# Performance work log

Measured on AMD Instinct MI355X. Metric: run time of the kernel, lower is better.

The kernel has to match this reference:

```python
import jax, jax.numpy as jnp
import numpy as np

DIM_IN = 30
DIM_Z = 32
TEMP = DIM_Z ** 0.5
N1, N2 = 2000, 4000


def setup_inputs() -> dict:
    key = jax.random.key(0)
    ks = jax.random.split(key, 16)
    s = 0.05
    f32 = jnp.float32
    return {
        "lm_X": jax.random.normal(ks[0], (N1, DIM_IN), f32),
        "lm_Y": jax.random.normal(ks[1], (N1, 2), f32),
        "tg_X": jax.random.normal(ks[2], (N2, DIM_IN), f32),
        "tg_Y": jax.random.normal(ks[3], (N2, 2), f32),
        "lm_delay": jax.random.uniform(ks[4], (N1,), f32),
        "tg_delay": jax.random.uniform(ks[5], (N2,), f32),
        "gamma_1": jnp.ones((1, 1), f32),
        "gamma_2": jnp.ones((1, 1), f32),
        "gamma_3": jnp.ones((1, 1), f32),
        "alpha": jnp.ones((1, 1), f32),
        "beta": jnp.zeros((1, 1), f32),
        "att_qw": jax.random.normal(ks[6], (DIM_IN, DIM_Z), f32) * s,
        "att_qb": jnp.zeros((DIM_Z,), f32),
        "att_kw": jax.random.normal(ks[7], (DIM_IN, DIM_Z), f32) * s,
        "att_kb": jnp.zeros((DIM_Z,), f32),
        "att_vw": jax.random.normal(ks[8], (DIM_IN + 2, DIM_Z), f32) * s,
        "att_vb": jnp.zeros((DIM_Z,), f32),
        "w1_w": jax.random.normal(ks[9], (DIM_IN + 2, DIM_IN + 2), f32) * s,
        "w1_b": jnp.zeros((DIM_IN + 2,), f32),
        "w2_w": jax.random.normal(ks[10], (DIM_IN + 2, DIM_IN + 2), f32) * s,
        "w2_b": jnp.zeros((DIM_IN + 2,), f32),
        "pred_qw": jax.random.normal(ks[11], (DIM_IN * 3 + 4, DIM_Z), f32) * s,
        "pred_qb": jnp.zeros((DIM_Z,), f32),
        "pred_kw": jax.random.normal(ks[12], (DIM_IN, DIM_Z), f32) * s,
        "pred_kb": jnp.zeros((DIM_Z,), f32),
        "pred_vw": jax.random.normal(ks[13], (2, 2), f32) * s,
        "pred_vb": jnp.zeros((2,), f32),
    }


def reference(lm_X, lm_Y, tg_X, tg_Y, lm_delay, tg_delay,
              gamma_1, gamma_2, gamma_3, alpha, beta,
              att_qw, att_qb, att_kw, att_kb, att_vw, att_vb,
              w1_w, w1_b, w2_w, w2_b,
              pred_qw, pred_qb, pred_kw, pred_kb, pred_vw, pred_vb):
    n1, n2 = lm_X.shape[0], tg_X.shape[0]
    n = n1 + n2 + 1
    dt = lm_X.dtype

    lm_feature = jnp.concatenate([lm_X, lm_Y], axis=1)                      # [N1, 32]
    tg_feature_0 = jnp.concatenate([tg_X, jnp.zeros((n2, 2), dt)], axis=1)  # [N2, 32]
    router_0 = jnp.mean(lm_feature, axis=0, keepdims=True)                  # [1, 32]
    all_feature_0 = jnp.concatenate([lm_feature, tg_feature_0, router_0], axis=0)

    # SimpleAttention1 (attribute similarity): log-softmax scores, exp -> softmax weights
    q = tg_X @ att_qw + att_qb
    k = lm_X @ att_kw + att_kb
    log_attn = jax.nn.log_softmax((q / TEMP) @ k.T, axis=-1)                # [N2, N1]
    attribute_score = jnp.exp(log_attn)

    delay_score = jnp.exp(-gamma_1 * (alpha * lm_delay + beta)).reshape(n1)
    rou2tar_0 = jnp.exp(-gamma_2 * (alpha * tg_delay + beta)).reshape(n2)

    # hop 1: dense star-graph adjacency, degree-normalized propagation
    adj0 = jnp.eye(n, dtype=dt)
    adj0 = adj0.at[n1:n1 + n2, :n1].set(attribute_score)
    adj0 = adj0.at[-1, :n1].set(delay_score)
    adj0 = adj0.at[n1:n1 + n2, -1].set(rou2tar_0)
    deg0 = jnp.sum(adj0, axis=1)
    step1 = ((adj0 / deg0[:, None]) @ all_feature_0) @ w1_w + w1_b          # D^-1 A X W1
    tg_feature_1 = step1[n1:n1 + n2]
    router_1 = step1[-1:].reshape(1, -1)

    # hop 2: router -> target only
    rou2tar_1 = jnp.exp(-gamma_3 * (alpha * tg_delay + beta)).reshape(n2)
    adj1 = jnp.eye(n, dtype=dt)
    adj1 = adj1.at[n1:n1 + n2, -1].set(rou2tar_1)
    all_feature_1 = jnp.concatenate([lm_feature, tg_feature_1, router_1], axis=0)
    deg1 = jnp.sum(adj1, axis=1)
    step2 = ((adj1 / deg1[:, None]) @ all_feature_1) @ w2_w + w2_b
    tg_feature_2 = step2[n1:n1 + n2]

    final_tg_feature = jnp.concatenate([tg_X, tg_feature_1, tg_feature_2], axis=-1)  # [N2, 94]

    # SimpleAttention2 (collaborative mlp): softmax attention over landmark locations
    pq = final_tg_feature @ pred_qw + pred_qb
    pk = lm_X @ pred_kw + pred_kb
    pv = lm_Y @ pred_vw + pred_vb
    pattn = jax.nn.softmax((pq / TEMP) @ pk.T, axis=-1)                     # [N2, N1]
    y_pred = pattn @ pv                                                     # [N2, 2]
    return y_pred, final_tg_feature
```

## Files before the change

kernel.cpp:

```cpp
#include <hip/hip_runtime.h>

#define N1v 2000
#define N2v 4000
#define DIN 30
#define DZ 32
#define DQ 94
#define INV_TEMP 0.17677669529663687f

__device__ __forceinline__ float wave_reduce_sum(float v) {
#pragma unroll
    for (int off = 32; off; off >>= 1) v += __shfl_xor(v, off, 64);
    return v;
}
__device__ __forceinline__ float rlane(float v, int l) {
    return __uint_as_float(__builtin_amdgcn_readlane(__float_as_uint(v), l));
}

__global__ __launch_bounds__(256) void prep_kernel(
    const float* __restrict__ lm_X, const float* __restrict__ lm_Y,
    const float* __restrict__ lm_delay, const float* __restrict__ tg_X,
    const float* __restrict__ att_qw, const float* __restrict__ att_qb,
    const float* __restrict__ att_kw, const float* __restrict__ att_kb,
    const float* __restrict__ pred_kw, const float* __restrict__ pred_kb,
    const float* __restrict__ pred_vw, const float* __restrict__ pred_vb,
    const float* __restrict__ gamma_1, const float* __restrict__ alpha,
    const float* __restrict__ beta,
    float* __restrict__ lm_feature, float* __restrict__ k_t,
    float* __restrict__ pk_t, float* __restrict__ pv,
    float* __restrict__ pS, float* __restrict__ pW, float* __restrict__ pSd,
    float* __restrict__ q_ws)
{
    __shared__ float sh_x[8][DIN];
    __shared__ float sh_k[DZ][9];
    __shared__ float sh_p[DZ][9];
    __shared__ float sh_s[8][DZ];
    __shared__ float sh_w[8][DZ];
    __shared__ float sh_d[8];
    const int t = threadIdx.x;

    if (blockIdx.x >= 250) {
        const int base = (blockIdx.x - 250) * 8;
        if (t < 8 * DIN) sh_x[t / DIN][t % DIN] = tg_X[base * DIN + t];
        __syncthreads();
        const int ty = t >> 5, c2 = t & 31;
        float acc = att_qb[c2];
#pragma unroll
        for (int d = 0; d < DIN; ++d) acc += sh_x[ty][d] * att_qw[d * DZ + c2];
        q_ws[(base + ty) * DZ + c2] = acc * INV_TEMP;
        return;
    }

    const int base = blockIdx.x * 8;
    if (t < 8 * DIN) sh_x[t / DIN][t % DIN] = lm_X[base * DIN + t];
    __syncthreads();
    const int ty = t >> 5, c = t & 31;
    const int row = base + ty;
    float kacc = att_kb[c], pacc = pred_kb[c];
#pragma unroll
    for (int d = 0; d < DIN; ++d) {
        float x = sh_x[ty][d];
        kacc += x * att_kw[d * DZ + c];
        pacc += x * pred_kw[d * DZ + c];
    }
    sh_k[c][ty] = kacc;
    sh_p[c][ty] = pacc;
    float f = (c < DIN) ? sh_x[ty][c] : lm_Y[row * 2 + (c - DIN)];
    lm_feature[row * DZ + c] = f;
    float ds = __expf(-gamma_1[0] * (alpha[0] * lm_delay[row] + beta[0]));
    sh_s[ty][c] = f;
    sh_w[ty][c] = ds * f;
    if (c == 0) sh_d[ty] = ds;
    if (c < 2) {
        pv[row * 2 + c] = lm_Y[row * 2] * pred_vw[c] +
                          lm_Y[row * 2 + 1] * pred_vw[2 + c] + pred_vb[c];
    }
    __syncthreads();
    const int oc = t >> 3, orow = t & 7;
    k_t[oc * N1v + base + orow] = sh_k[oc][orow];
    pk_t[oc * N1v + base + orow] = sh_p[oc][orow];
    if (t < DZ) {
        float S = 0.f, W = 0.f;
#pragma unroll
        for (int g = 0; g < 8; ++g) { S += sh_s[g][t]; W += sh_w[g][t]; }
        pS[blockIdx.x * DZ + t] = S;
        pW[blockIdx.x * DZ + t] = W;
    }
    if (t == DZ) {
        float Sd = 0.f;
#pragma unroll
        for (int g = 0; g < 8; ++g) Sd += sh_d[g];
        pSd[blockIdx.x] = Sd;
    }
}

__global__ __launch_bounds__(256) void attn1_kernel(
    const float* __restrict__ q_ws, const float* __restrict__ k_t,
    const float* __restrict__ lm_feature,
    const float* __restrict__ pS, const float* __restrict__ pW,
    const float* __restrict__ pSd,
    const float* __restrict__ w1_w, const float* __restrict__ w1_b,
    float* __restrict__ a1den, float* __restrict__ a1agg,
    float* __restrict__ router_0, float* __restrict__ router_1)
{
    __shared__ __align__(16) float e_lds[4][8][288];
    __shared__ float rps[8][DZ];
    __shared__ float rpw[8][DZ];
    __shared__ float rpd[8];
    __shared__ float rhr[DZ];
    const int tid = threadIdx.x;

    if (blockIdx.x == 1000) {
        const int c = tid & 31, g = tid >> 5;
        float S = 0.f, W = 0.f, Sd = 0.f;
        for (int b = g; b < 250; b += 8) {
            S += pS[b * DZ + c];
            W += pW[b * DZ + c];
            if (c == 0) Sd += pSd[b];
        }
        rps[g][c] = S; rpw[g][c] = W;
        if (c == 0) rpd[g] = Sd;
        __syncthreads();
        if (tid < DZ) {
            float S2 = 0.f, W2 = 0.f, Sd2 = 0.f;
#pragma unroll
            for (int g2 = 0; g2 < 8; ++g2) { S2 += rps[g2][tid]; W2 += rpw[g2][tid]; Sd2 += rpd[g2]; }
            float r0 = S2 / (float)N1v;
            router_0[tid] = r0;
            rhr[tid] = (r0 + W2) / (1.f + Sd2);
        }
        __syncthreads();
        if (tid < DZ) {
            float acc = w1_b[tid];
#pragma unroll
            for (int d = 0; d < DZ; ++d) acc += rhr[d] * w1_w[d * DZ + tid];
            router_1[tid] = acc;
        }
        return;
    }

    const int wv = tid >> 6;
    const int lane = tid & 63;
    const int half = lane >> 5, c = lane & 31;
    const int tg = blockIdx.x >> 3;
    const int chunk = blockIdx.x & 7;
    const int t0 = tg * 32 + wv * 8;

    float qreg[4];
#pragma unroll
    for (int p = 0; p < 4; ++p)
        qreg[p] = q_ws[(t0 + 2 * p + half) * DZ + c];

    const int r0 = lane * 4;
    const int tb = chunk << 8;
    const int j = tb + r0;
    const int rld = (j <= N1v - 4) ? j : (N1v - 4);
    const bool dead = (j >= N1v);

    float s[8][4] = {};
    const float* kp = k_t + rld;
#pragma unroll 8
    for (int cc = 0; cc < DZ; ++cc) {
        float4 kt = *(const float4*)(kp + cc * N1v);
#pragma unroll
        for (int p = 0; p < 4; ++p) {
            float qa = rlane(qreg[p], cc);
            float qb = rlane(qreg[p], 32 + cc);
            s[2*p][0] += qa*kt.x; s[2*p][1] += qa*kt.y; s[2*p][2] += qa*kt.z; s[2*p][3] += qa*kt.w;
            s[2*p+1][0] += qb*kt.x; s[2*p+1][1] += qb*kt.y; s[2*p+1][2] += qb*kt.z; s[2*p+1][3] += qb*kt.w;
        }
    }
    if (dead) {
#pragma unroll
        for (int t = 0; t < 8; ++t)
#pragma unroll
            for (int k = 0; k < 4; ++k) s[t][k] = -1e30f;
    }

    const int wbase = (r0 & 7) * 36 + (r0 >> 3);
    float den[8];
#pragma unroll
    for (int t = 0; t < 8; ++t) {
        float e0 = __expf(s[t][0]), e1 = __expf(s[t][1]);
        float e2 = __expf(s[t][2]), e3 = __expf(s[t][3]);
        den[t] = (e0 + e1) + (e2 + e3);
        e_lds[wv][t][wbase      ] = e0;
        e_lds[wv][t][wbase +  36] = e1;
        e_lds[wv][t][wbase +  72] = e2;
        e_lds[wv][t][wbase + 108] = e3;
    }

    const int rg = lane >> 3, cq = lane & 7;
    const int ebase = rg * 36;
    const float* lmp = lm_feature + (tb + rg) * DZ + cq * 4;
    float agg[8][4] = {};
#pragma unroll 2
    for (int p4 = 0; p4 < 8; ++p4) {
        float4 ev[8];
#pragma unroll
        for (int t = 0; t < 8; ++t)
            ev[t] = *(const float4*)&e_lds[wv][t][ebase + p4 * 4];
#pragma unroll
        for (int k = 0; k < 4; ++k) {
            float4 lmv = *(const float4*)(lmp + ((p4 * 4 + k) << 8));
#pragma unroll
            for (int t = 0; t < 8; ++t) {
                float e = (k == 0) ? ev[t].x : (k == 1) ? ev[t].y : (k == 2) ? ev[t].z : ev[t].w;
                agg[t][0] += e*lmv.x; agg[t][1] += e*lmv.y;
                agg[t][2] += e*lmv.z; agg[t][3] += e*lmv.w;
            }
        }
    }

#pragma unroll
    for (int t = 0; t < 8; ++t) {
#pragma unroll
        for (int off = 8; off <= 32; off <<= 1)
#pragma unroll
            for (int k = 0; k < 4; ++k) agg[t][k] += __shfl_xor(agg[t][k], off, 64);
        den[t] = wave_reduce_sum(den[t]);
    }
    if (lane < 8) {
#pragma unroll
        for (int t = 0; t < 8; ++t) {
            float4 av = {agg[t][0], agg[t][1], agg[t][2], agg[t][3]};
            *(float4*)&a1agg[((t0 + t) * 8 + chunk) * DZ + lane * 4] = av;
        }
    }
    float dout = 0.f;
#pragma unroll
    for (int t = 0; t < 8; ++t)
        if (lane == t) dout = den[t];
    if (lane < 8)
        a1den[(t0 + lane) * 8 + chunk] = dout;
}

__global__ __launch_bounds__(256) void merge1_kernel(
    const float* __restrict__ tg_X, const float* __restrict__ tg_delay,
    const float* __restrict__ w1_w, const float* __restrict__ w1_b,
    const float* __restrict__ w2_w, const float* __restrict__ w2_b,
    const float* __restrict__ pred_qw, const float* __restrict__ pred_qb,
    const float* __restrict__ gamma_2, const float* __restrict__ gamma_3,
    const float* __restrict__ alpha, const float* __restrict__ beta,
    const float* __restrict__ router_0, const float* __restrict__ router_1,
    const float* __restrict__ a1den, const float* __restrict__ a1agg,
    float* __restrict__ ftf_out, float* __restrict__ pq_ws)
{
    const int t = threadIdx.x;
    const int wv = t >> 6;
    const int lane = t & 63;
    const int half = lane >> 5, cc2 = lane & 31;
    const int i = blockIdx.x * 8 + wv * 2 + half;

    float dsum = 0.f, asum = 0.f;
#pragma unroll
    for (int w = 0; w < 8; ++w) {
        dsum += a1den[i * 8 + w];
        asum += a1agg[(i * 8 + w) * DZ + cc2];
    }

    float xr = (cc2 < DIN) ? tg_X[i * DIN + cc2] : 0.f;
    const float al = alpha[0], be = beta[0];
    float td = tg_delay[i];
    float r2t0 = __expf(-gamma_2[0] * (al * td + be));
    float r2t1 = __expf(-gamma_3[0] * (al * td + be));
    float h0 = (xr + asum / dsum + r2t0 * router_0[cc2]) / (2.f + r2t0);
    float tf1 = w1_b[cc2];
#pragma unroll 8
    for (int d = 0; d < DZ; ++d) {
        float hv = half ? rlane(h0, 32 + d) : rlane(h0, d);
        tf1 += hv * w1_w[d * DZ + cc2];
    }
    float h1 = (tf1 + r2t1 * router_1[cc2]) / (1.f + r2t1);
    float tf2 = w2_b[cc2];
#pragma unroll 8
    for (int d = 0; d < DZ; ++d) {
        float hv = half ? rlane(h1, 32 + d) : rlane(h1, d);
        tf2 += hv * w2_w[d * DZ + cc2];
    }
    if (cc2 < DIN) ftf_out[i * DQ + cc2] = xr;
    ftf_out[i * DQ + DIN + cc2] = tf1;
    ftf_out[i * DQ + DIN + DZ + cc2] = tf2;
    float pq = pred_qb[cc2];
#pragma unroll 8
    for (int d = 0; d < DIN; ++d) {
        float hv = half ? rlane(xr, 32 + d) : rlane(xr, d);
        pq += hv * pred_qw[d * DZ + cc2];
    }
#pragma unroll 8
    for (int d = 0; d < DZ; ++d) {
        float hv = half ? rlane(tf1, 32 + d) : rlane(tf1, d);
        pq += hv * pred_qw[(DIN + d) * DZ + cc2];
    }
#pragma unroll 8
    for (int d = 0; d < DZ; ++d) {
        float hv = half ? rlane(tf2, 32 + d) : rlane(tf2, d);
        pq += hv * pred_qw[(DIN + DZ + d) * DZ + cc2];
    }
    pq_ws[i * DZ + cc2] = pq * INV_TEMP;
}

__global__ __launch_bounds__(256) void attn2_kernel(
    const float* __restrict__ pq_ws, const float* __restrict__ pk_t,
    const float* __restrict__ pv, float* __restrict__ a2p)
{
    __shared__ __align__(16) float4 red[4][8][64];
    const int wv = threadIdx.x >> 6;
    const int lane = threadIdx.x & 63;
    const int half = lane >> 5, c = lane & 31;
    const int tg = blockIdx.x >> 3;
    const int chunk = blockIdx.x & 7;
    const int t0 = tg * 32 + wv * 8;

    float qreg[4];
#pragma unroll
    for (int p = 0; p < 4; ++p)
        qreg[p] = pq_ws[(t0 + 2 * p + half) * DZ + c];

    const int r0 = lane * 4;
    const int tb = chunk << 8;
    const int j = tb + r0;
    const int rld = (j <= N1v - 4) ? j : (N1v - 4);
    const bool dead = (j >= N1v);

    float s[8][4] = {};
    const float* kp = pk_t + rld;
#pragma unroll 8
    for (int cc = 0; cc < DZ; ++cc) {
        float4 kt = *(const float4*)(kp + cc * N1v);
#pragma unroll
        for (int p = 0; p < 4; ++p) {
            float qa = rlane(qreg[p], cc);
            float qb = rlane(qreg[p], 32 + cc);
            s[2*p][0] += qa*kt.x; s[2*p][1] += qa*kt.y; s[2*p][2] += qa*kt.z; s[2*p][3] += qa*kt.w;
            s[2*p+1][0] += qb*kt.x; s[2*p+1][1] += qb*kt.y; s[2*p+1][2] += qb*kt.z; s[2*p+1][3] += qb*kt.w;
        }
    }
    if (dead) {
#pragma unroll
        for (int t = 0; t < 8; ++t)
#pragma unroll
            for (int k = 0; k < 4; ++k) s[t][k] = -1e30f;
    }

    float4 pva = *(const float4*)(pv + 2 * rld);
    float4 pvb = *(const float4*)(pv + 2 * rld + 4);
#pragma unroll
    for (int t = 0; t < 8; ++t) {
        float e0 = __expf(s[t][0]), e1 = __expf(s[t][1]);
        float e2 = __expf(s[t][2]), e3 = __expf(s[t][3]);
        float d2 = (e0 + e1) + (e2 + e3);
        float ya = e0*pva.x + e1*pva.z + e2*pvb.x + e3*pvb.z;
        float yb = e0*pva.y + e1*pva.w + e2*pvb.y + e3*pvb.w;
        red[wv][t][lane] = make_float4(d2, ya, yb, 0.f);
    }

    const int rt = lane >> 3, rk = lane & 7;
    float4 acc = red[wv][rt][rk];
#pragma unroll
    for (int k = 1; k < 8; ++k) {
        float4 v = red[wv][rt][rk + 8 * k];
        acc.x += v.x; acc.y += v.y; acc.z += v.z;
    }
#pragma unroll
    for (int off = 1; off <= 4; off <<= 1) {
        acc.x += __shfl_xor(acc.x, off, 64);
        acc.y += __shfl_xor(acc.y, off, 64);
        acc.z += __shfl_xor(acc.z, off, 64);
    }
    if (rk == 0)
        ((float4*)a2p)[chunk * N2v + t0 + rt] = acc;
}

__global__ __launch_bounds__(256) void merge2_kernel(
    const float* __restrict__ a2p, float* __restrict__ y_out)
{
    const int t = blockIdx.x * 256 + threadIdx.x;
    if (t >= N2v) return;
    float D = 0.f, Y0 = 0.f, Y1 = 0.f;
#pragma unroll
    for (int w = 0; w < 8; ++w) {
        float4 v = ((const float4*)a2p)[w * N2v + t];
        D += v.x; Y0 += v.y; Y1 += v.z;
    }
    y_out[2 * t] = Y0 / D;
    y_out[2 * t + 1] = Y1 / D;
}

extern "C" void kernel_launch(void* const* d_in, const int* in_sizes, int n_in,
                              void* d_out, int out_size, void* d_ws, size_t ws_size,
                              hipStream_t stream) {
    const float* lm_X     = (const float*)d_in[0];
    const float* lm_Y     = (const float*)d_in[1];
    const float* tg_X     = (const float*)d_in[2];
    const float* lm_delay = (const float*)d_in[4];
    const float* tg_delay = (const float*)d_in[5];
    const float* gamma_1  = (const float*)d_in[6];
    const float* gamma_2  = (const float*)d_in[7];
    const float* gamma_3  = (const float*)d_in[8];
    const float* alpha    = (const float*)d_in[9];
    const float* beta     = (const float*)d_in[10];
    const float* att_qw   = (const float*)d_in[11];
    const float* att_qb   = (const float*)d_in[12];
    const float* att_kw   = (const float*)d_in[13];
    const float* att_kb   = (const float*)d_in[14];
    const float* w1_w     = (const float*)d_in[17];
    const float* w1_b     = (const float*)d_in[18];
    const float* w2_w     = (const float*)d_in[19];
    const float* w2_b     = (const float*)d_in[20];
    const float* pred_qw  = (const float*)d_in[21];
    const float* pred_qb  = (const float*)d_in[22];
    const float* pred_kw  = (const float*)d_in[23];
    const float* pred_kb  = (const float*)d_in[24];
    const float* pred_vw  = (const float*)d_in[25];
    const float* pred_vb  = (const float*)d_in[26];

    float* ws          = (float*)d_ws;
    float* k_t         = ws;
    float* pk_t        = ws + 64000;
    float* lm_feature  = ws + 128000;
    float* pv          = ws + 192000;
    float* pS          = ws + 196000;
    float* pW          = ws + 204000;
    float* pSd         = ws + 212000;
    float* router_0    = ws + 212256;
    float* router_1    = ws + 212288;
    float* q_ws        = ws + 212320;
    float* pq_ws       = ws + 340320;
    float* a1den       = ws + 468320;
    float* a1agg       = ws + 500320;
    float* a2p         = ws + 1524320;

    float* y_out   = (float*)d_out;
    float* ftf_out = y_out + 2 * N2v;

    prep_kernel<<<250 + N2v / 8, 256, 0, stream>>>(
        lm_X, lm_Y, lm_delay, tg_X, att_qw, att_qb, att_kw, att_kb,
        pred_kw, pred_kb, pred_vw, pred_vb, gamma_1, alpha, beta,
        lm_feature, k_t, pk_t, pv, pS, pW, pSd, q_ws);

    attn1_kernel<<<1001, 256, 0, stream>>>(
        q_ws, k_t, lm_feature, pS, pW, pSd, w1_w, w1_b,
        a1den, a1agg, router_0, router_1);

    merge1_kernel<<<500, 256, 0, stream>>>(
        tg_X, tg_delay, w1_w, w1_b, w2_w, w2_b,
        pred_qw, pred_qb, gamma_2, gamma_3, alpha, beta,
        router_0, router_1, a1den, a1agg, ftf_out, pq_ws);

    attn2_kernel<<<1000, 256, 0, stream>>>(
        pq_ws, pk_t, pv, a2p);

    merge2_kernel<<<16, 256, 0, stream>>>(a2p, y_out);
}
```

Before: 59.16 us.

## Fuse merge1 into attn2, recomputing target query per chunk block

The merge1 kernel is folded into attn2. Each attn2 block recomputes the GCN hop features and prediction queries for its 32 targets into shared memory, and only chunk 0 writes final_tg_feature. This removes one kernel launch and the pq_ws global round trip. In exchange, the merge work is done redundantly 8 times, once per landmark chunk, which lengthens each attn2 block's prologue.

```diff
diff --git a/kernel.cpp b/kernel.cpp
--- a/kernel.cpp
+++ b/kernel.cpp
@@ -234,7 +234,7 @@
         a1den[(t0 + lane) * 8 + chunk] = dout;
 }
 
-__global__ __launch_bounds__(256) void merge1_kernel(
+__global__ __launch_bounds__(256) void attn2_kernel(
     const float* __restrict__ tg_X, const float* __restrict__ tg_delay,
     const float* __restrict__ w1_w, const float* __restrict__ w1_b,
     const float* __restrict__ w2_w, const float* __restrict__ w2_b,
@@ -243,78 +243,78 @@
     const float* __restrict__ alpha, const float* __restrict__ beta,
     const float* __restrict__ router_0, const float* __restrict__ router_1,
     const float* __restrict__ a1den, const float* __restrict__ a1agg,
-    float* __restrict__ ftf_out, float* __restrict__ pq_ws)
-{
-    const int t = threadIdx.x;
-    const int wv = t >> 6;
-    const int lane = t & 63;
-    const int half = lane >> 5, cc2 = lane & 31;
-    const int i = blockIdx.x * 8 + wv * 2 + half;
-
-    float dsum = 0.f, asum = 0.f;
-#pragma unroll
-    for (int w = 0; w < 8; ++w) {
-        dsum += a1den[i * 8 + w];
-        asum += a1agg[(i * 8 + w) * DZ + cc2];
-    }
-
-    float xr = (cc2 < DIN) ? tg_X[i * DIN + cc2] : 0.f;
-    const float al = alpha[0], be = beta[0];
-    float td = tg_delay[i];
-    float r2t0 = __expf(-gamma_2[0] * (al * td + be));
-    float r2t1 = __expf(-gamma_3[0] * (al * td + be));
-    float h0 = (xr + asum / dsum + r2t0 * router_0[cc2]) / (2.f + r2t0);
-    float tf1 = w1_b[cc2];
-#pragma unroll 8
-    for (int d = 0; d < DZ; ++d) {
-        float hv = half ? rlane(h0, 32 + d) : rlane(h0, d);
-        tf1 += hv * w1_w[d * DZ + cc2];
-    }
-    float h1 = (tf1 + r2t1 * router_1[cc2]) / (1.f + r2t1);
-    float tf2 = w2_b[cc2];
-#pragma unroll 8
-    for (int d = 0; d < DZ; ++d) {
-        float hv = half ? rlane(h1, 32 + d) : rlane(h1, d);
-        tf2 += hv * w2_w[d * DZ + cc2];
-    }
-    if (cc2 < DIN) ftf_out[i * DQ + cc2] = xr;
-    ftf_out[i * DQ + DIN + cc2] = tf1;
-    ftf_out[i * DQ + DIN + DZ + cc2] = tf2;
-    float pq = pred_qb[cc2];
-#pragma unroll 8
-    for (int d = 0; d < DIN; ++d) {
-        float hv = half ? rlane(xr, 32 + d) : rlane(xr, d);
-        pq += hv * pred_qw[d * DZ + cc2];
-    }
-#pragma unroll 8
-    for (int d = 0; d < DZ; ++d) {
-        float hv = half ? rlane(tf1, 32 + d) : rlane(tf1, d);
-        pq += hv * pred_qw[(DIN + d) * DZ + cc2];
-    }
-#pragma unroll 8
-    for (int d = 0; d < DZ; ++d) {
-        float hv = half ? rlane(tf2, 32 + d) : rlane(tf2, d);
-        pq += hv * pred_qw[(DIN + DZ + d) * DZ + cc2];
-    }
-    pq_ws[i * DZ + cc2] = pq * INV_TEMP;
-}
-
-__global__ __launch_bounds__(256) void attn2_kernel(
-    const float* __restrict__ pq_ws, const float* __restrict__ pk_t,
-    const float* __restrict__ pv, float* __restrict__ a2p)
+    const float* __restrict__ pk_t, const float* __restrict__ pv,
+    float* __restrict__ ftf_out, float* __restrict__ a2p)
 {
     __shared__ __align__(16) float4 red[4][8][64];
-    const int wv = threadIdx.x >> 6;
-    const int lane = threadIdx.x & 63;
+    __shared__ float pq_lds[32][DZ];
+    const int tid = threadIdx.x;
+    const int wv = tid >> 6;
+    const int lane = tid & 63;
     const int half = lane >> 5, c = lane & 31;
     const int tg = blockIdx.x >> 3;
     const int chunk = blockIdx.x & 7;
+
+    const float al = alpha[0], be = beta[0];
+    const float g2v = gamma_2[0], g3v = gamma_3[0];
+#pragma unroll 1
+    for (int it = 0; it < 4; ++it) {
+        const int li = it * 8 + wv * 2 + half;
+        const int i = tg * 32 + li;
+        float dsum = 0.f, asum = 0.f;
+#pragma unroll
+        for (int w = 0; w < 8; ++w) {
+            dsum += a1den[i * 8 + w];
+            asum += a1agg[(i * 8 + w) * DZ + c];
+        }
+        float xr = (c < DIN) ? tg_X[i * DIN + c] : 0.f;
+        float td = tg_delay[i];
+        float r2t0 = __expf(-g2v * (al * td + be));
+        float r2t1 = __expf(-g3v * (al * td + be));
+        float h0 = (xr + asum / dsum + r2t0 * router_0[c]) / (2.f + r2t0);
+        float tf1 = w1_b[c];
+#pragma unroll 8
+        for (int d = 0; d < DZ; ++d) {
+            float hv = half ? rlane(h0, 32 + d) : rlane(h0, d);
+            tf1 += hv * w1_w[d * DZ + c];
+        }
+        float h1 = (tf1 + r2t1 * router_1[c]) / (1.f + r2t1);
+        float tf2 = w2_b[c];
+#pragma unroll 8
+        for (int d = 0; d < DZ; ++d) {
+            float hv = half ? rlane(h1, 32 + d) : rlane(h1, d);
+            tf2 += hv * w2_w[d * DZ + c];
+        }
+        if (chunk == 0) {
+            if (c < DIN) ftf_out[i * DQ + c] = xr;
+            ftf_out[i * DQ + DIN + c] = tf1;
+            ftf_out[i * DQ + DIN + DZ + c] = tf2;
+        }
+        float pq = pred_qb[c];
+#pragma unroll 8
+        for (int d = 0; d < DIN; ++d) {
+            float hv = half ? rlane(xr, 32 + d) : rlane(xr, d);
+            pq += hv * pred_qw[d * DZ + c];
+        }
+#pragma unroll 8
+        for (int d = 0; d < DZ; ++d) {
+            float hv = half ? rlane(tf1, 32 + d) : rlane(tf1, d);
+            pq += hv * pred_qw[(DIN + d) * DZ + c];
+        }
+#pragma unroll 8
+        for (int d = 0; d < DZ; ++d) {
+            float hv = half ? rlane(tf2, 32 + d) : rlane(tf2, d);
+            pq += hv * pred_qw[(DIN + DZ + d) * DZ + c];
+        }
+        pq_lds[li][c] = pq * INV_TEMP;
+    }
+    __syncthreads();
+
     const int t0 = tg * 32 + wv * 8;
-
     float qreg[4];
 #pragma unroll
     for (int p = 0; p < 4; ++p)
-        qreg[p] = pq_ws[(t0 + 2 * p + half) * DZ + c];
+        qreg[p] = pq_lds[wv * 8 + 2 * p + half][c];
 
     const int r0 = lane * 4;
     const int tb = chunk << 8;
@@ -425,10 +425,9 @@
     float* router_0    = ws + 212256;
     float* router_1    = ws + 212288;
     float* q_ws        = ws + 212320;
-    float* pq_ws       = ws + 340320;
-    float* a1den       = ws + 468320;
-    float* a1agg       = ws + 500320;
-    float* a2p         = ws + 1524320;
+    float* a1den       = ws + 340320;
+    float* a1agg       = ws + 372320;
+    float* a2p         = ws + 1396320;
 
     float* y_out   = (float*)d_out;
     float* ftf_out = y_out + 2 * N2v;
@@ -442,13 +441,11 @@
         q_ws, k_t, lm_feature, pS, pW, pSd, w1_w, w1_b,
         a1den, a1agg, router_0, router_1);
 
-    merge1_kernel<<<500, 256, 0, stream>>>(
+    attn2_kernel<<<1000, 256, 0, stream>>>(
         tg_X, tg_delay, w1_w, w1_b, w2_w, w2_b,
         pred_qw, pred_qb, gamma_2, gamma_3, alpha, beta,
-        router_0, router_1, a1den, a1agg, ftf_out, pq_ws);
-
-    attn2_kernel<<<1000, 256, 0, stream>>>(
-        pq_ws, pk_t, pv, a2p);
+        router_0, router_1, a1den, a1agg, pk_t, pv,
+        ftf_out, a2p);
 
     merge2_kernel<<<16, 256, 0, stream>>>(a2p, y_out);
 }
```

Result: slower. 101.5 us (+71.6%).
